# Kernel optimization log

Hardware: AMD Instinct MI355X
Metric: run time of the kernel (lower is better)

Reference implementation:

```python
import jax, jax.numpy as jnp
import numpy as np

B, N, E = 2, 5000, 160000
F_IN, HID, ED = 128, 128, 16
IN_EDGE = 2 * F_IN + 16 + ED  # source, target, radial(4*4), edge_attr


def _lin(k, fan_in, fan_out):
    return (jax.random.normal(k, (fan_in, fan_out), jnp.float32) / np.sqrt(fan_in)).astype(jnp.float32)


def setup_inputs() -> dict:
    key = jax.random.key(0)
    ks = jax.random.split(key, 16)
    h = jax.random.normal(ks[0], (B, N, F_IN), jnp.float32)
    coord = jax.random.normal(ks[1], (B, N, 4, 3), jnp.float32)
    edge_index = jax.random.randint(ks[2], (2, E), 0, N)
    edge_attr = jax.random.normal(ks[3], (E, ED), jnp.float32)
    return {
        "h": h, "coord": coord, "edge_index": edge_index, "edge_attr": edge_attr,
        # edge_mlp: Linear(IN_EDGE->HID), ReLU, Linear(HID->HID), ReLU
        "W_e1": _lin(ks[4], IN_EDGE, HID), "b_e1": jnp.zeros((HID,), jnp.float32),
        "W_e2": _lin(ks[5], HID, HID), "b_e2": jnp.zeros((HID,), jnp.float32),
        # node_mlp: Linear(HID+F_IN->HID), ReLU, Linear(HID->F_IN)
        "W_n1": _lin(ks[6], HID + F_IN, HID), "b_n1": jnp.zeros((HID,), jnp.float32),
        "W_n2": _lin(ks[7], HID, F_IN), "b_n2": jnp.zeros((F_IN,), jnp.float32),
        # coord_mlp: Linear(HID->HID), ReLU, Linear(HID->4, bias=False, xavier gain 0.001)
        "W_c1": _lin(ks[8], HID, HID), "b_c1": jnp.zeros((HID,), jnp.float32),
        "W_c2": _lin(ks[9], HID, 4) * 0.001,
    }


def reference(h, coord, edge_index, edge_attr,
              W_e1, b_e1, W_e2, b_e2,
              W_n1, b_n1, W_n2, b_n2,
              W_c1, b_c1, W_c2):
    row, col = edge_index[0], edge_index[1]
    coords_weight = 1.0
    n_nodes = h.shape[1]

    def single(h_b, coord_b):
        # coord2radial
        cd = coord_b[row] - coord_b[col]                                  # [E,4,3]
        prod = jnp.einsum('ejt,ekt->ejk', cd, cd).reshape(cd.shape[0], -1)  # [E,16]
        nrm = jnp.linalg.norm(prod, axis=-1, keepdims=True)
        radial = prod / jnp.maximum(nrm, 1e-12)                           # F.normalize
        # edge_model
        x = jnp.concatenate([h_b[row], h_b[col], radial, edge_attr], axis=-1)
        ef = jax.nn.relu(jax.nn.relu(x @ W_e1 + b_e1) @ W_e2 + b_e2)      # [E,HID]
        # coord_model: segment mean of cd * coord_mlp(ef)
        w = jax.nn.relu(ef @ W_c1 + b_c1) @ W_c2                          # [E,4]
        trans = cd * w[:, :, None]                                        # [E,4,3]
        agg_c = jax.ops.segment_sum(trans, row, num_segments=n_nodes)     # [N,4,3]
        cnt = jax.ops.segment_sum(jnp.ones((row.shape[0],), trans.dtype), row,
                                  num_segments=n_nodes)                   # [N]
        coord_new = coord_b + (agg_c / jnp.maximum(cnt, 1.0)[:, None, None]) * coords_weight
        # node_model (recurrent)
        agg_h = jax.ops.segment_sum(ef, row, num_segments=n_nodes)        # [N,HID]
        z = jnp.concatenate([h_b, agg_h], axis=-1)
        h_new = h_b + jax.nn.relu(z @ W_n1 + b_n1) @ W_n2 + b_n2
        return h_new, coord_new

    hs, coords = jax.vmap(single)(h, coord)
    return hs, coords
```

## Files before the change

kernel.cpp:

```cpp
#include <hip/hip_runtime.h>
#include <hip/hip_bf16.h>

#define B   2
#define NN_ 5000
#define NE_ 160000
#define F   128
#define HID 128
#define ED  16

typedef __bf16 bf16x8 __attribute__((ext_vector_type(8)));
typedef __bf16 bf16x4 __attribute__((ext_vector_type(4)));
typedef float  f32x4  __attribute__((ext_vector_type(4)));

#define MS  136
#define PS  40
#define EDG 128
#define ZS  264
#define HS  136
#define NPB2 32

__global__ void pack_weights(const float* __restrict__ We1, const float* __restrict__ We2,
                             const float* __restrict__ Wc1, const float* __restrict__ Wc2,
                             const float* __restrict__ Wn1, const float* __restrict__ Wn2,
                             __bf16* __restrict__ pw1, __bf16* __restrict__ pw2,
                             __bf16* __restrict__ pwc1, __bf16* __restrict__ pwc2,
                             __bf16* __restrict__ pwn1, __bf16* __restrict__ pwn2)
{
    int idx = blockIdx.x * 256 + threadIdx.x;
    const float* W; __bf16* P; int KT, Nr, local;
    if (idx < 36864)       { W = We1; P = pw1;  KT = 9; Nr = 128; local = idx; }
    else if (idx < 53248)  { W = We2; P = pw2;  KT = 4; Nr = 128; local = idx - 36864; }
    else if (idx < 69632)  { W = Wc1; P = pwc1; KT = 4; Nr = 128; local = idx - 53248; }
    else if (idx < 71680)  { W = Wc2; P = pwc2; KT = 4; Nr = 4;   local = idx - 69632; }
    else if (idx < 104448) { W = Wn1; P = pwn1; KT = 8; Nr = 128; local = idx - 71680; }
    else                   { W = Wn2; P = pwn2; KT = 4; Nr = 128; local = idx - 104448; }
    int j = local & 7, lane = (local >> 3) & 63, rest = local >> 9;
    int kt = rest % KT, nt = rest / KT;
    int k = kt * 32 + (lane >> 4) * 8 + j;
    int n = nt * 16 + (lane & 15);
    float v = (n < Nr) ? W[k * Nr + n] : 0.f;
    P[local] = (__bf16)v;
}

__global__ void hist_kernel(const int* __restrict__ ei, int* __restrict__ csr_cnt)
{
    int i = blockIdx.x * 256 + threadIdx.x;
    if (i < NE_) atomicAdd(&csr_cnt[ei[i]], 1);
}

__global__ void scan_kernel(const int* __restrict__ csr_cnt,
                            int* __restrict__ csr_off, int* __restrict__ csr_pos)
{
    __shared__ int part[256];
    const int t = threadIdx.x;
    int sum = 0;
    #pragma unroll
    for (int j = 0; j < 20; j++) {
        int idx = t * 20 + j;
        if (idx < NN_) sum += csr_cnt[idx];
    }
    part[t] = sum;
    __syncthreads();
    if (t == 0) {
        int run = 0;
        for (int i = 0; i < 256; i++) { int v = part[i]; part[i] = run; run += v; }
    }
    __syncthreads();
    int run = part[t];
    #pragma unroll
    for (int j = 0; j < 20; j++) {
        int idx = t * 20 + j;
        if (idx < NN_) { csr_off[idx] = run; csr_pos[idx] = run; run += csr_cnt[idx]; }
    }
    if (t == 0) csr_off[NN_] = NE_;
}

__global__ void bucket_kernel(const int* __restrict__ ei, const float* __restrict__ ea,
                              int* __restrict__ csr_pos, int* __restrict__ bucket,
                              __bf16* __restrict__ eas)
{
    int i = blockIdx.x * 256 + threadIdx.x;
    if (i < NE_) {
        int p = atomicAdd(&csr_pos[ei[i]], 1);
        bucket[p] = i;
        const float4* src = (const float4*)(ea + (size_t)i * ED);
        __bf16* dst = eas + (size_t)p * ED;
        #pragma unroll
        for (int j = 0; j < 4; j++) {
            float4 v = src[j];
            bf16x4 bv = {(__bf16)v.x, (__bf16)v.y, (__bf16)v.z, (__bf16)v.w};
            *(bf16x4*)&dst[j * 4] = bv;
        }
    }
}

__global__ __launch_bounds__(512) void pre_kernel(
    const float* __restrict__ h, const __bf16* __restrict__ pw1,
    __bf16* __restrict__ pr, __bf16* __restrict__ pc)
{
    __shared__ __align__(16) __bf16 hs[128 * MS];
    const int t = threadIdx.x;
    const int b = blockIdx.y;
    const int n0 = blockIdx.x * 128;
    const int lane = t & 63, wave = t >> 6;
    const int quad = lane >> 4, c = lane & 15;

    #pragma unroll
    for (int it = 0; it < 8; it++) {
        int idx = it * 512 + t;
        int node = idx >> 5, ch = idx & 31;
        int gn = n0 + node;
        float4 v = (gn < NN_) ? *(const float4*)&h[((size_t)b * NN_ + gn) * F + ch * 4]
                              : (float4){0.f, 0.f, 0.f, 0.f};
        bf16x4 bv = {(__bf16)v.x, (__bf16)v.y, (__bf16)v.z, (__bf16)v.w};
        *(bf16x4*)&hs[node * MS + ch * 4] = bv;
    }
    __syncthreads();

    const bf16x8* pw1v = (const bf16x8*)pw1;
    f32x4 accr[8], accc[8];
    #pragma unroll
    for (int m = 0; m < 8; m++) { accr[m] = (f32x4){0,0,0,0}; accc[m] = (f32x4){0,0,0,0}; }
    for (int kt = 0; kt < 4; kt++) {
        bf16x8 wr = pw1v[(wave * 9 + kt) * 64 + lane];
        bf16x8 wc = pw1v[(wave * 9 + kt + 4) * 64 + lane];
        #pragma unroll
        for (int m = 0; m < 8; m++) {
            bf16x8 x = *(const bf16x8*)&hs[(m * 16 + c) * MS + kt * 32 + quad * 8];
            accr[m] = __builtin_amdgcn_mfma_f32_16x16x32_bf16(wr, x, accr[m], 0, 0, 0);
            accc[m] = __builtin_amdgcn_mfma_f32_16x16x32_bf16(wc, x, accc[m], 0, 0, 0);
        }
    }
    #pragma unroll
    for (int m = 0; m < 8; m++) {
        int gn = n0 + m * 16 + c;
        if (gn < NN_) {
            size_t base = ((size_t)b * NN_ + gn) * F + wave * 16 + quad * 4;
            bf16x4 orr = {(__bf16)accr[m][0], (__bf16)accr[m][1], (__bf16)accr[m][2], (__bf16)accr[m][3]};
            bf16x4 occ = {(__bf16)accc[m][0], (__bf16)accc[m][1], (__bf16)accc[m][2], (__bf16)accc[m][3]};
            *(bf16x4*)&pr[base] = orr;
            *(bf16x4*)&pc[base] = occ;
        }
    }
}

__global__ __launch_bounds__(512, 4) void edge_kernel(
    const __bf16* __restrict__ pr, const __bf16* __restrict__ pc,
    const float* __restrict__ coord,
    const int* __restrict__ ei, const __bf16* __restrict__ eas,
    const int* __restrict__ bucket,
    const float* __restrict__ be1, const float* __restrict__ be2,
    const float* __restrict__ bc1,
    const __bf16* __restrict__ pw1, const __bf16* __restrict__ pw2,
    const __bf16* __restrict__ pwc1, const __bf16* __restrict__ pwc2,
    float* __restrict__ agg_h, float* __restrict__ agg_c)
{
    __shared__ __align__(16) __bf16 buf1[EDG * MS];
    __shared__ __align__(16) __bf16 buf2[EDG * MS];
    __shared__ __bf16 cds[EDG][12];
    __shared__ int rs[EDG], cs[EDG];

    const int t = threadIdx.x;
    const int b = blockIdx.y;
    const int p0 = blockIdx.x * EDG;
    const int lane = t & 63, wave = t >> 6;
    const int quad = lane >> 4, c = lane & 15;
    const int mh = wave >> 2, np = wave & 3;

    if (t < EDG) {
        int eid = bucket[p0 + t];
        rs[t] = ei[eid]; cs[t] = ei[NE_ + eid];
    }
    __syncthreads();

    const __bf16* prb = pr + (size_t)b * NN_ * F;
    const __bf16* pcb = pc + (size_t)b * NN_ * F;
    #pragma unroll
    for (int it = 0; it < 4; it++) {
        int idx = it * 512 + t;
        int e = idx >> 4, ch = idx & 15;
        bf16x8 a = *(const bf16x8*)(prb + (size_t)rs[e] * F + ch * 8);
        bf16x8 v = *(const bf16x8*)(pcb + (size_t)cs[e] * F + ch * 8);
        bf16x8 o;
        #pragma unroll
        for (int j = 0; j < 8; j++) o[j] = (__bf16)((float)a[j] + (float)v[j]);
        *(bf16x8*)&buf1[e * MS + ch * 8] = o;
    }
    if (t < EDG) {
        int e = t;
        const float* cr = coord + ((size_t)b * NN_ + rs[e]) * 12;
        const float* cc = coord + ((size_t)b * NN_ + cs[e]) * 12;
        float cd[12];
        #pragma unroll
        for (int j = 0; j < 12; j++) { cd[j] = cr[j] - cc[j]; cds[e][j] = (__bf16)cd[j]; }
        float prod[16]; float ss = 0.f;
        #pragma unroll
        for (int j = 0; j < 4; j++)
            #pragma unroll
            for (int k = 0; k < 4; k++) {
                float p = cd[j*3]*cd[k*3] + cd[j*3+1]*cd[k*3+1] + cd[j*3+2]*cd[k*3+2];
                prod[j*4 + k] = p; ss += p * p;
            }
        float inv = 1.0f / fmaxf(sqrtf(ss), 1e-12f);
        #pragma unroll
        for (int j = 0; j < 16; j++) buf2[e * PS + j] = (__bf16)(prod[j] * inv);
        const uint4* ep = (const uint4*)(eas + (size_t)(p0 + e) * 16);
        *(uint4*)&buf2[e * PS + 16] = ep[0];
        *(uint4*)&buf2[e * PS + 24] = ep[1];
    }
    __syncthreads();

    const bf16x8* pw1v  = (const bf16x8*)pw1;
    const bf16x8* pw2v  = (const bf16x8*)pw2;
    const bf16x8* pwc1v = (const bf16x8*)pwc1;
    const bf16x8* pwc2v = (const bf16x8*)pwc2;

    f32x4 acc1[4][2];
    #pragma unroll
    for (int m = 0; m < 4; m++)
        #pragma unroll
        for (int n = 0; n < 2; n++) acc1[m][n] = (f32x4){0,0,0,0};
    {
        bf16x8 x1[4];
        #pragma unroll
        for (int m = 0; m < 4; m++)
            x1[m] = *(const bf16x8*)&buf2[((mh*4 + m)*16 + c) * PS + quad*8];
        #pragma unroll
        for (int n = 0; n < 2; n++) {
            bf16x8 w = pw1v[((2*np + n)*9 + 8)*64 + lane];
            #pragma unroll
            for (int m = 0; m < 4; m++)
                acc1[m][n] = __builtin_amdgcn_mfma_f32_16x16x32_bf16(w, x1[m], acc1[m][n], 0, 0, 0);
        }
    }
    #pragma unroll
    for (int n = 0; n < 2; n++) {
        int nt = 2*np + n;
        float4 bb = *(const float4*)&be1[nt*16 + quad*4];
        #pragma unroll
        for (int m = 0; m < 4; m++) {
            int row = (mh*4 + m)*16 + c;
            bf16x4 p = *(const bf16x4*)&buf1[row * MS + nt*16 + quad*4];
            bf16x4 o = { (__bf16)fmaxf(acc1[m][n][0] + (float)p[0] + bb.x, 0.f),
                         (__bf16)fmaxf(acc1[m][n][1] + (float)p[1] + bb.y, 0.f),
                         (__bf16)fmaxf(acc1[m][n][2] + (float)p[2] + bb.z, 0.f),
                         (__bf16)fmaxf(acc1[m][n][3] + (float)p[3] + bb.w, 0.f) };
            *(bf16x4*)&buf1[row * MS + nt*16 + quad*4] = o;
        }
    }
    __syncthreads();

    f32x4 acc2[4][2];
    #pragma unroll
    for (int m = 0; m < 4; m++)
        #pragma unroll
        for (int n = 0; n < 2; n++) acc2[m][n] = (f32x4){0,0,0,0};
    for (int kt = 0; kt < 4; kt++) {
        bf16x8 x[4];
        #pragma unroll
        for (int m = 0; m < 4; m++)
            x[m] = *(const bf16x8*)&buf1[((mh*4 + m)*16 + c) * MS + kt*32 + quad*8];
        #pragma unroll
        for (int n = 0; n < 2; n++) {
            bf16x8 w = pw2v[((2*np + n)*4 + kt)*64 + lane];
            #pragma unroll
            for (int m = 0; m < 4; m++)
                acc2[m][n] = __builtin_amdgcn_mfma_f32_16x16x32_bf16(w, x[m], acc2[m][n], 0, 0, 0);
        }
    }
    #pragma unroll
    for (int n = 0; n < 2; n++) {
        int nt = 2*np + n;
        float4 bb = *(const float4*)&be2[nt*16 + quad*4];
        #pragma unroll
        for (int m = 0; m < 4; m++) {
            int row = (mh*4 + m)*16 + c;
            bf16x4 o = { (__bf16)fmaxf(acc2[m][n][0] + bb.x, 0.f),
                         (__bf16)fmaxf(acc2[m][n][1] + bb.y, 0.f),
                         (__bf16)fmaxf(acc2[m][n][2] + bb.z, 0.f),
                         (__bf16)fmaxf(acc2[m][n][3] + bb.w, 0.f) };
            *(bf16x4*)&buf2[row * MS + nt*16 + quad*4] = o;
        }
    }
    __syncthreads();

    f32x4 acc3[4][2];
    #pragma unroll
    for (int m = 0; m < 4; m++)
        #pragma unroll
        for (int n = 0; n < 2; n++) acc3[m][n] = (f32x4){0,0,0,0};
    for (int kt = 0; kt < 4; kt++) {
        bf16x8 x[4];
        #pragma unroll
        for (int m = 0; m < 4; m++)
            x[m] = *(const bf16x8*)&buf2[((mh*4 + m)*16 + c) * MS + kt*32 + quad*8];
        #pragma unroll
        for (int n = 0; n < 2; n++) {
            bf16x8 w = pwc1v[((2*np + n)*4 + kt)*64 + lane];
            #pragma unroll
            for (int m = 0; m < 4; m++)
                acc3[m][n] = __builtin_amdgcn_mfma_f32_16x16x32_bf16(w, x[m], acc3[m][n], 0, 0, 0);
        }
    }
    #pragma unroll
    for (int n = 0; n < 2; n++) {
        int nt = 2*np + n;
        float4 bb = *(const float4*)&bc1[nt*16 + quad*4];
        #pragma unroll
        for (int m = 0; m < 4; m++) {
            int row = (mh*4 + m)*16 + c;
            bf16x4 o = { (__bf16)fmaxf(acc3[m][n][0] + bb.x, 0.f),
                         (__bf16)fmaxf(acc3[m][n][1] + bb.y, 0.f),
                         (__bf16)fmaxf(acc3[m][n][2] + bb.z, 0.f),
                         (__bf16)fmaxf(acc3[m][n][3] + bb.w, 0.f) };
            *(bf16x4*)&buf1[row * MS + nt*16 + quad*4] = o;
        }
    }
    __syncthreads();

    f32x4 accw = (f32x4){0,0,0,0};
    for (int kt = 0; kt < 4; kt++) {
        bf16x8 x = *(const bf16x8*)&buf1[(wave*16 + c) * MS + kt*32 + quad*8];
        accw = __builtin_amdgcn_mfma_f32_16x16x32_bf16(pwc2v[kt*64 + lane], x, accw, 0, 0, 0);
    }
    if (quad == 0) {
        int e = wave*16 + c;
        #pragma unroll
        for (int j = 0; j < 12; j++)
            cds[e][j] = (__bf16)((float)cds[e][j] * accw[j/3]);
    }
    __syncthreads();

    {
        float* aggh_b = agg_h + (size_t)b * NN_ * HID;
        const int col = t & 127, seg = t >> 7;
        float run = 0.f;
        int cur = rs[seg * 32];
        for (int e = seg * 32; e < seg * 32 + 32; e++) {
            int r = rs[e];
            float v = (float)buf2[e * MS + col];
            if (r != cur) {
                atomicAdd(&aggh_b[(size_t)cur * HID + col], run);
                run = 0.f; cur = r;
            }
            run += v;
        }
        atomicAdd(&aggh_b[(size_t)cur * HID + col], run);
    }
    if (t < 96) {
        float* aggc_b = agg_c + (size_t)b * NN_ * 12;
        const int j = t % 12, q = t / 12;
        float run = 0.f;
        int cur = rs[q * 16];
        for (int e = q * 16; e < q * 16 + 16; e++) {
            int r = rs[e];
            float v = (float)cds[e][j];
            if (r != cur) {
                atomicAdd(&aggc_b[(size_t)cur * 12 + j], run);
                run = 0.f; cur = r;
            }
            run += v;
        }
        atomicAdd(&aggc_b[(size_t)cur * 12 + j], run);
    }
}

__global__ __launch_bounds__(256) void node_kernel(
    const float* __restrict__ h, const float* __restrict__ agg_h,
    const float* __restrict__ agg_c, const float* __restrict__ coord,
    const int* __restrict__ csr_off,
    const __bf16* __restrict__ pwn1, const float* __restrict__ bn1,
    const __bf16* __restrict__ pwn2, const float* __restrict__ bn2,
    float* __restrict__ out_h, float* __restrict__ out_c)
{
    __shared__ __align__(16) __bf16 zs[NPB2 * ZS];
    __shared__ __align__(16) __bf16 h1s[NPB2 * HS];
    const int t = threadIdx.x;
    const int b = blockIdx.y;
    const int n0 = blockIdx.x * NPB2;
    const int lane = t & 63, wave = t >> 6;
    const int quad = lane >> 4, c = lane & 15;

    #pragma unroll
    for (int it = 0; it < 8; it++) {
        int idx = it * 256 + t;
        int node = idx >> 6, ch = idx & 63;
        int gn = n0 + node;
        float4 v = (float4){0.f, 0.f, 0.f, 0.f};
        if (gn < NN_) {
            const float* src = (ch < 32) ? &h[((size_t)b * NN_ + gn) * F + ch * 4]
                                         : &agg_h[((size_t)b * NN_ + gn) * HID + (ch - 32) * 4];
            v = *(const float4*)src;
        }
        bf16x4 bv = {(__bf16)v.x, (__bf16)v.y, (__bf16)v.z, (__bf16)v.w};
        *(bf16x4*)&zs[node * ZS + ch * 4] = bv;
    }
    __syncthreads();

    const bf16x8* w1v = (const bf16x8*)pwn1;
    const bf16x8* w2v = (const bf16x8*)pwn2;
    f32x4 a1[2][2];
    #pragma unroll
    for (int m = 0; m < 2; m++)
        #pragma unroll
        for (int n = 0; n < 2; n++) a1[m][n] = (f32x4){0,0,0,0};
    for (int kt = 0; kt < 8; kt++) {
        bf16x8 x[2];
        #pragma unroll
        for (int m = 0; m < 2; m++)
            x[m] = *(const bf16x8*)&zs[(m*16 + c) * ZS + kt*32 + quad*8];
        #pragma unroll
        for (int n = 0; n < 2; n++) {
            bf16x8 w = w1v[((2*wave + n)*8 + kt)*64 + lane];
            #pragma unroll
            for (int m = 0; m < 2; m++)
                a1[m][n] = __builtin_amdgcn_mfma_f32_16x16x32_bf16(w, x[m], a1[m][n], 0, 0, 0);
        }
    }
    __syncthreads();
    #pragma unroll
    for (int n = 0; n < 2; n++) {
        int nt = 2*wave + n;
        float4 bb = *(const float4*)&bn1[nt*16 + quad*4];
        #pragma unroll
        for (int m = 0; m < 2; m++) {
            bf16x4 o = { (__bf16)fmaxf(a1[m][n][0] + bb.x, 0.f),
                         (__bf16)fmaxf(a1[m][n][1] + bb.y, 0.f),
                         (__bf16)fmaxf(a1[m][n][2] + bb.z, 0.f),
                         (__bf16)fmaxf(a1[m][n][3] + bb.w, 0.f) };
            *(bf16x4*)&h1s[(m*16 + c) * HS + nt*16 + quad*4] = o;
        }
    }
    __syncthreads();

    f32x4 a2[2][2];
    #pragma unroll
    for (int m = 0; m < 2; m++)
        #pragma unroll
        for (int n = 0; n < 2; n++) a2[m][n] = (f32x4){0,0,0,0};
    for (int kt = 0; kt < 4; kt++) {
        bf16x8 x[2];
        #pragma unroll
        for (int m = 0; m < 2; m++)
            x[m] = *(const bf16x8*)&h1s[(m*16 + c) * HS + kt*32 + quad*8];
        #pragma unroll
        for (int n = 0; n < 2; n++) {
            bf16x8 w = w2v[((2*wave + n)*4 + kt)*64 + lane];
            #pragma unroll
            for (int m = 0; m < 2; m++)
                a2[m][n] = __builtin_amdgcn_mfma_f32_16x16x32_bf16(w, x[m], a2[m][n], 0, 0, 0);
        }
    }
    float* os = (float*)zs;
    #pragma unroll
    for (int n = 0; n < 2; n++) {
        int nt = 2*wave + n;
        float4 bb = *(const float4*)&bn2[nt*16 + quad*4];
        #pragma unroll
        for (int m = 0; m < 2; m++) {
            f32x4 o = { a2[m][n][0] + bb.x, a2[m][n][1] + bb.y,
                        a2[m][n][2] + bb.z, a2[m][n][3] + bb.w };
            *(f32x4*)&os[(m*16 + c) * 132 + nt*16 + quad*4] = o;
        }
    }
    __syncthreads();

    #pragma unroll
    for (int it = 0; it < 4; it++) {
        int idx = it * 256 + t;
        int node = idx >> 5, ch = idx & 31;
        int gn = n0 + node;
        if (gn < NN_) {
            size_t gb = ((size_t)b * NN_ + gn) * F + ch * 4;
            float4 hres = *(const float4*)&h[gb];
            float4 acc = *(const float4*)&os[node * 132 + ch * 4];
            float4 o = { hres.x + acc.x, hres.y + acc.y, hres.z + acc.z, hres.w + acc.w };
            *(float4*)&out_h[gb] = o;
        }
    }
    for (int idx = t; idx < NPB2 * 12; idx += 256) {
        int node = idx / 12, j = idx % 12;
        int gn = n0 + node;
        if (gn < NN_) {
            float deg = (float)(csr_off[gn + 1] - csr_off[gn]);
            size_t ci = ((size_t)b * NN_ + gn) * 12 + j;
            out_c[ci] = coord[ci] + agg_c[ci] / fmaxf(deg, 1.0f);
        }
    }
}

extern "C" void kernel_launch(void* const* d_in, const int* in_sizes, int n_in,
                              void* d_out, int out_size, void* d_ws, size_t ws_size,
                              hipStream_t stream) {
    const float* h     = (const float*)d_in[0];
    const float* coord = (const float*)d_in[1];
    const int*   ei    = (const int*)d_in[2];
    const float* ea    = (const float*)d_in[3];
    const float* We1   = (const float*)d_in[4];
    const float* be1   = (const float*)d_in[5];
    const float* We2   = (const float*)d_in[6];
    const float* be2   = (const float*)d_in[7];
    const float* Wn1   = (const float*)d_in[8];
    const float* bn1   = (const float*)d_in[9];
    const float* Wn2   = (const float*)d_in[10];
    const float* bn2   = (const float*)d_in[11];
    const float* Wc1   = (const float*)d_in[12];
    const float* bc1   = (const float*)d_in[13];
    const float* Wc2   = (const float*)d_in[14];

    float* out_h = (float*)d_out;
    float* out_c = out_h + (size_t)B * NN_ * F;

    unsigned char* base = (unsigned char*)d_ws;
    __bf16* pw1  = (__bf16*)base;
    __bf16* pw2  = pw1 + 36864;
    __bf16* pwc1 = pw2 + 16384;
    __bf16* pwc2 = pwc1 + 16384;
    __bf16* pwn1 = pwc2 + 2048;
    __bf16* pwn2 = pwn1 + 32768;
    unsigned char* dyn = base + 241664;

    int* csr_cnt = (int*)(dyn);
    int* csr_off = (int*)(dyn + 20000);
    int* csr_pos = (int*)(dyn + 40016);
    int* bucket  = (int*)(dyn + 60016);
    float* agg_h = (float*)(dyn + 700016);
    float* agg_c = agg_h + (size_t)B * NN_ * HID;
    __bf16* pr   = (__bf16*)(agg_c + (size_t)B * NN_ * 12);
    __bf16* pc   = pr + (size_t)B * NN_ * F;
    __bf16* eas  = pc + (size_t)B * NN_ * F;

    pack_weights<<<472, 256, 0, stream>>>(We1, We2, Wc1, Wc2, Wn1, Wn2,
                                          pw1, pw2, pwc1, pwc2, pwn1, pwn2);

    hipMemsetAsync(csr_cnt, 0, 20000, stream);
    hipMemsetAsync(agg_h, 0, (size_t)B * NN_ * (HID + 12) * sizeof(float), stream);

    hist_kernel<<<625, 256, 0, stream>>>(ei, csr_cnt);
    scan_kernel<<<1, 256, 0, stream>>>(csr_cnt, csr_off, csr_pos);
    bucket_kernel<<<625, 256, 0, stream>>>(ei, ea, csr_pos, bucket, eas);

    dim3 pg((NN_ + 127) / 128, B);
    pre_kernel<<<pg, 512, 0, stream>>>(h, pw1, pr, pc);

    dim3 eg(NE_ / EDG, B);
    edge_kernel<<<eg, 512, 0, stream>>>(pr, pc, coord, ei, eas, bucket, be1, be2, bc1,
                                        pw1, pw2, pwc1, pwc2, agg_h, agg_c);

    dim3 ng((NN_ + NPB2 - 1) / NPB2, B);
    node_kernel<<<ng, 256, 0, stream>>>(h, agg_h, agg_c, coord, csr_off,
                                        pwn1, bn1, pwn2, bn2, out_h, out_c);
}
```

Baseline: 208.5 us.

## Fold memsets into pack kernel, merge bucket and pre kernels, pair agg_h reduction

The two hipMemsetAsync calls are removed and their zeroing is done inside pack_weights, and bucket_kernel and pre_kernel are merged into one launch whose blocks are split by blockIdx. This removes several launches and serialization points, so the bucketing and the node pre-projection can run at the same time. The agg_h segmented reduction in edge_kernel now has each thread handle two adjacent bf16 columns over 16 edges, where before it handled one column over 32. That changes the mix of LDS reads and atomics, and it assumes the pack grid's stride covers the zeroed region.

Result: faster. 203.9 us (-2.2%).

```diff
diff --git a/kernel.cpp b/kernel.cpp
--- a/kernel.cpp
+++ b/kernel.cpp
@@ -18,13 +18,15 @@
 #define ZS  264
 #define HS  136
 #define NPB2 32
+#define NBUCKET 313
 
 __global__ void pack_weights(const float* __restrict__ We1, const float* __restrict__ We2,
                              const float* __restrict__ Wc1, const float* __restrict__ Wc2,
                              const float* __restrict__ Wn1, const float* __restrict__ Wn2,
                              __bf16* __restrict__ pw1, __bf16* __restrict__ pw2,
                              __bf16* __restrict__ pwc1, __bf16* __restrict__ pwc2,
-                             __bf16* __restrict__ pwn1, __bf16* __restrict__ pwn2)
+                             __bf16* __restrict__ pwn1, __bf16* __restrict__ pwn2,
+                             float4* __restrict__ agg4, int* __restrict__ csr_cnt)
 {
     int idx = blockIdx.x * 256 + threadIdx.x;
     const float* W; __bf16* P; int KT, Nr, local;
@@ -40,6 +42,10 @@
     int n = nt * 16 + (lane & 15);
     float v = (n < Nr) ? W[k * Nr + n] : 0.f;
     P[local] = (__bf16)v;
+
+    float4 z4 = {0.f, 0.f, 0.f, 0.f};
+    for (int i = idx; i < 350000; i += 120832) agg4[i] = z4;
+    if (idx < NN_) csr_cnt[idx] = 0;
 }
 
 __global__ void hist_kernel(const int* __restrict__ ei, int* __restrict__ csr_cnt)
@@ -75,33 +81,35 @@
     if (t == 0) csr_off[NN_] = NE_;
 }
 
-__global__ void bucket_kernel(const int* __restrict__ ei, const float* __restrict__ ea,
-                              int* __restrict__ csr_pos, int* __restrict__ bucket,
-                              __bf16* __restrict__ eas)
-{
-    int i = blockIdx.x * 256 + threadIdx.x;
-    if (i < NE_) {
-        int p = atomicAdd(&csr_pos[ei[i]], 1);
-        bucket[p] = i;
-        const float4* src = (const float4*)(ea + (size_t)i * ED);
-        __bf16* dst = eas + (size_t)p * ED;
-        #pragma unroll
-        for (int j = 0; j < 4; j++) {
-            float4 v = src[j];
-            bf16x4 bv = {(__bf16)v.x, (__bf16)v.y, (__bf16)v.z, (__bf16)v.w};
-            *(bf16x4*)&dst[j * 4] = bv;
-        }
-    }
-}
-
-__global__ __launch_bounds__(512) void pre_kernel(
+__global__ __launch_bounds__(512) void mid_kernel(
+    const int* __restrict__ ei, const float* __restrict__ ea,
+    int* __restrict__ csr_pos, int* __restrict__ bucket, __bf16* __restrict__ eas,
     const float* __restrict__ h, const __bf16* __restrict__ pw1,
     __bf16* __restrict__ pr, __bf16* __restrict__ pc)
 {
     __shared__ __align__(16) __bf16 hs[128 * MS];
     const int t = threadIdx.x;
-    const int b = blockIdx.y;
-    const int n0 = blockIdx.x * 128;
+
+    if (blockIdx.x < NBUCKET) {
+        int i = blockIdx.x * 512 + t;
+        if (i < NE_) {
+            int p = atomicAdd(&csr_pos[ei[i]], 1);
+            bucket[p] = i;
+            const float4* src = (const float4*)(ea + (size_t)i * ED);
+            __bf16* dst = eas + (size_t)p * ED;
+            #pragma unroll
+            for (int j = 0; j < 4; j++) {
+                float4 v = src[j];
+                bf16x4 bv = {(__bf16)v.x, (__bf16)v.y, (__bf16)v.z, (__bf16)v.w};
+                *(bf16x4*)&dst[j * 4] = bv;
+            }
+        }
+        return;
+    }
+
+    const int bp = blockIdx.x - NBUCKET;
+    const int b = bp / 40;
+    const int n0 = (bp % 40) * 128;
     const int lane = t & 63, wave = t >> 6;
     const int quad = lane >> 4, c = lane & 15;
 
@@ -333,19 +341,24 @@
 
     {
         float* aggh_b = agg_h + (size_t)b * NN_ * HID;
-        const int col = t & 127, seg = t >> 7;
-        float run = 0.f;
-        int cur = rs[seg * 32];
-        for (int e = seg * 32; e < seg * 32 + 32; e++) {
+        const int cp = t & 63;
+        const int seg = t >> 6;
+        float r0 = 0.f, r1 = 0.f;
+        int cur = rs[seg * 16];
+        for (int e = seg * 16; e < seg * 16 + 16; e++) {
             int r = rs[e];
-            float v = (float)buf2[e * MS + col];
+            unsigned u = *(const unsigned*)&buf2[e * MS + cp * 2];
+            float v0 = __uint_as_float(u << 16);
+            float v1 = __uint_as_float(u & 0xffff0000u);
             if (r != cur) {
-                atomicAdd(&aggh_b[(size_t)cur * HID + col], run);
-                run = 0.f; cur = r;
+                atomicAdd(&aggh_b[(size_t)cur * HID + cp*2],     r0);
+                atomicAdd(&aggh_b[(size_t)cur * HID + cp*2 + 1], r1);
+                r0 = r1 = 0.f; cur = r;
             }
-            run += v;
-        }
-        atomicAdd(&aggh_b[(size_t)cur * HID + col], run);
+            r0 += v0; r1 += v1;
+        }
+        atomicAdd(&aggh_b[(size_t)cur * HID + cp*2],     r0);
+        atomicAdd(&aggh_b[(size_t)cur * HID + cp*2 + 1], r1);
     }
     if (t < 96) {
         float* aggc_b = agg_c + (size_t)b * NN_ * 12;
@@ -531,17 +544,14 @@
     __bf16* eas  = pc + (size_t)B * NN_ * F;
 
     pack_weights<<<472, 256, 0, stream>>>(We1, We2, Wc1, Wc2, Wn1, Wn2,
-                                          pw1, pw2, pwc1, pwc2, pwn1, pwn2);
-
-    hipMemsetAsync(csr_cnt, 0, 20000, stream);
-    hipMemsetAsync(agg_h, 0, (size_t)B * NN_ * (HID + 12) * sizeof(float), stream);
+                                          pw1, pw2, pwc1, pwc2, pwn1, pwn2,
+                                          (float4*)agg_h, csr_cnt);
 
     hist_kernel<<<625, 256, 0, stream>>>(ei, csr_cnt);
     scan_kernel<<<1, 256, 0, stream>>>(csr_cnt, csr_off, csr_pos);
-    bucket_kernel<<<625, 256, 0, stream>>>(ei, ea, csr_pos, bucket, eas);
-
-    dim3 pg((NN_ + 127) / 128, B);
-    pre_kernel<<<pg, 512, 0, stream>>>(h, pw1, pr, pc);
+
+    mid_kernel<<<NBUCKET + 80, 512, 0, stream>>>(ei, ea, csr_pos, bucket, eas,
+                                                 h, pw1, pr, pc);
 
     dim3 eg(NE_ / EDG, B);
     edge_kernel<<<eg, 512, 0, stream>>>(pr, pc, coord, ei, eas, bucket, be1, be2, bc1,
```
